# Performance work log

Hardware: AMD Instinct MI355X
Metric: run time of the kernel (lower is better)

The kernel has to match this reference:

```python
import jax, jax.numpy as jnp
import numpy as np

B, NV, L, NKG = 8, 100, 128, 923
NT = NV + 1 + NKG  # 1024 total nodes
DV, DK, DH, H, NLAYERS, VOCAB = 2048, 300, 1024, 8, 3, 50265
DHD = DH // H


def _ln(x, g, b, eps=1e-5):
    m = x.mean(-1, keepdims=True)
    v = x.var(-1, keepdims=True)
    return (x - m) / jnp.sqrt(v + eps) * g + b


def _gat_layer(x, mask, W, bb, a_src, a_dst, ln_g, ln_b):
    # x: [B,N,D], mask: [B,N,N] bool
    Bn, N, D = x.shape
    h = (x @ W + bb).reshape(Bn, N, H, DHD)
    s = jnp.einsum('bnhd,hd->bnh', h, a_src)  # source term
    t = jnp.einsum('bnhd,hd->bnh', h, a_dst)  # target term
    e = jax.nn.leaky_relu(s[:, :, None, :] + t[:, None, :, :], 0.2)  # [B,N,N,H]
    e = jnp.where(mask[..., None], e, -1e9)
    a = jax.nn.softmax(e, axis=2)  # over neighbors j
    out = jnp.einsum('bijh,bjhd->bihd', a, h).reshape(Bn, N, D)
    return _ln(x + out, ln_g, ln_b)


def setup_inputs() -> dict:
    key = jax.random.key(0)
    ks = jax.random.split(key, 24)
    s = 0.02
    inp = {
        'visual_features': jax.random.normal(ks[0], (B, NV, DV), jnp.float32),
        'question_input_ids': jax.random.randint(ks[1], (B, L), 0, VOCAB, jnp.int64) if False else jax.random.randint(ks[1], (B, L), 0, VOCAB).astype(jnp.int32),
        'question_attention_mask': jnp.ones((B, L), jnp.int32),
        'graph_node_features': jax.random.normal(ks[2], (B, NKG, DK), jnp.float32),
        'graph_adj': jax.random.randint(ks[3], (B, NT, NT), 0, 2).astype(jnp.int32),
        'graph_node_types': jax.random.randint(ks[4], (B, NT), 0, 3).astype(jnp.int32),
        # params
        'vis_W': jax.random.normal(ks[5], (DV, DH), jnp.float32) * s,
        'vis_b': jnp.zeros((DH,), jnp.float32),
        'vis_ln_g': jnp.ones((DH,), jnp.float32),
        'vis_ln_b': jnp.zeros((DH,), jnp.float32),
        'tok_emb': jax.random.normal(ks[6], (VOCAB, DH), jnp.float32) * s,
        'q_W': jax.random.normal(ks[7], (DH, DH), jnp.float32) * s,
        'q_b': jnp.zeros((DH,), jnp.float32),
        'q_ln_g': jnp.ones((DH,), jnp.float32),
        'q_ln_b': jnp.zeros((DH,), jnp.float32),
        'kg_W': jax.random.normal(ks[8], (DK, DH), jnp.float32) * s,
        'kg_b': jnp.zeros((DH,), jnp.float32),
        'kg_ln_g': jnp.ones((DH,), jnp.float32),
        'kg_ln_b': jnp.zeros((DH,), jnp.float32),
        'type_emb': jax.random.normal(ks[9], (3, DH), jnp.float32) * s,
        'gat_W': jax.random.normal(ks[10], (NLAYERS, DH, DH), jnp.float32) * s,
        'gat_b': jnp.zeros((NLAYERS, DH), jnp.float32),
        'a_src': jax.random.normal(ks[11], (NLAYERS, H, DHD), jnp.float32) * s,
        'a_dst': jax.random.normal(ks[12], (NLAYERS, H, DHD), jnp.float32) * s,
        'gat_ln_g': jnp.ones((NLAYERS, DH), jnp.float32),
        'gat_ln_b': jnp.zeros((NLAYERS, DH), jnp.float32),
        'readout_W': jax.random.normal(ks[13], (DH, 1), jnp.float32) * s,
        'readout_b': jnp.zeros((1,), jnp.float32),
        'cs_W1': jax.random.normal(ks[14], (DH, DH), jnp.float32) * s,
        'cs_b1': jnp.zeros((DH,), jnp.float32),
        'cs_W2': jax.random.normal(ks[15], (DH, 1), jnp.float32) * s,
        'cs_b2': jnp.zeros((1,), jnp.float32),
    }
    return inp


def reference(visual_features, question_input_ids, question_attention_mask,
              graph_node_features, graph_adj, graph_node_types,
              vis_W, vis_b, vis_ln_g, vis_ln_b,
              tok_emb, q_W, q_b, q_ln_g, q_ln_b,
              kg_W, kg_b, kg_ln_g, kg_ln_b,
              type_emb, gat_W, gat_b, a_src, a_dst, gat_ln_g, gat_ln_b,
              readout_W, readout_b, cs_W1, cs_b1, cs_W2, cs_b2):
    # 1. visual projection
    vis = _ln(visual_features @ vis_W + vis_b, vis_ln_g, vis_ln_b)  # [B,NV,DH]
    # 2. text encoder (embedding + masked mean-pool + proj + LN)
    te = tok_emb[question_input_ids]  # [B,L,DH]
    m = question_attention_mask.astype(te.dtype)[..., None]
    pooled = (te * m).sum(1) / jnp.maximum(m.sum(1), 1.0)
    q = _ln(pooled @ q_W + q_b, q_ln_g, q_ln_b)[:, None, :]  # [B,1,DH]
    # 3. KG projection
    kg = _ln(graph_node_features @ kg_W + kg_b, kg_ln_g, kg_ln_b)
    # 4-5. concat + node-type embeddings
    x = jnp.concatenate([vis, q, kg], axis=1) + type_emb[graph_node_types]
    # 6. dense GAT stack
    mask = graph_adj > 0
    for l in range(NLAYERS):
        x = _gat_layer(x, mask, gat_W[l], gat_b[l], a_src[l], a_dst[l],
                       gat_ln_g[l], gat_ln_b[l])
    # 7. attention-pooled readout
    w = jax.nn.softmax((x @ readout_W + readout_b).squeeze(-1), axis=-1)
    g = (x * w[..., None]).sum(1)  # [B,DH]
    # 8. candidate scorer
    logits = jax.nn.gelu(g @ cs_W1 + cs_b1) @ cs_W2 + cs_b2  # [B,1]
    return logits
```

## Files before the change

kernel.cpp:

```cpp
#include <hip/hip_runtime.h>
#include <math.h>

#define NB 8
#define NV 100
#define LQ 128
#define NKG 923
#define NT 1024
#define DV 2048
#define DK 300
#define DH 1024
#define NH 8
#define DHD 128
#define NLAYERS 3

typedef __attribute__((ext_vector_type(8))) short short8;
typedef __attribute__((ext_vector_type(4))) float f32x4;

__device__ __forceinline__ short f2bf(float f) {
    unsigned u = __float_as_uint(f);
    u += 0x7fff + ((u >> 16) & 1);
    return (short)(u >> 16);
}
__device__ __forceinline__ float bf2f(short s) {
    unsigned u = ((unsigned)(unsigned short)s) << 16;
    return __uint_as_float(u);
}
__device__ __forceinline__ unsigned pack2(float a, float b) {
    return (unsigned)(unsigned short)f2bf(a) | ((unsigned)(unsigned short)f2bf(b) << 16);
}

#if __has_builtin(__builtin_amdgcn_global_load_lds)
#define HAVE_GLL 1
__device__ __forceinline__ void gll16(const void* g, void* l) {
    __builtin_amdgcn_global_load_lds(
        (const __attribute__((address_space(1))) void*)g,
        (__attribute__((address_space(3))) void*)l, 16, 0, 0);
}
#else
#define HAVE_GLL 0
#endif

__device__ __forceinline__ float block_sum1(float a, float* red4) {
#pragma unroll
    for (int off = 32; off > 0; off >>= 1) a += __shfl_xor(a, off, 64);
    int w = threadIdx.x >> 6;
    if ((threadIdx.x & 63) == 0) red4[w] = a;
    __syncthreads();
    return red4[0] + red4[1] + red4[2] + red4[3];
}
__device__ __forceinline__ float block_max1(float a, float* red4) {
#pragma unroll
    for (int off = 32; off > 0; off >>= 1) a = fmaxf(a, __shfl_xor(a, off, 64));
    int w = threadIdx.x >> 6;
    if ((threadIdx.x & 63) == 0) red4[w] = a;
    __syncthreads();
    return fmaxf(fmaxf(red4[0], red4[1]), fmaxf(red4[2], red4[3]));
}
__device__ __forceinline__ float2 block_sum2(float a, float b, float* red8) {
#pragma unroll
    for (int off = 32; off > 0; off >>= 1) {
        a += __shfl_xor(a, off, 64);
        b += __shfl_xor(b, off, 64);
    }
    int w = threadIdx.x >> 6;
    if ((threadIdx.x & 63) == 0) { red8[w] = a; red8[4 + w] = b; }
    __syncthreads();
    float2 r;
    r.x = red8[0] + red8[1] + red8[2] + red8[3];
    r.y = red8[4] + red8[5] + red8[6] + red8[7];
    return r;
}

__global__ __launch_bounds__(256) void bitmask_kernel(
    const int* __restrict__ adj, unsigned* __restrict__ mb)
{
    int bi = blockIdx.x;
    int tid = threadIdx.x;
#pragma unroll
    for (int p = 0; p < 4; ++p) {
        int j = p * 256 + tid;
        unsigned long long bal = __ballot(adj[(size_t)bi * NT + j] > 0);
        if ((tid & 63) == 0) {
            int w = (p * 256 + (tid & 0xC0)) >> 5;
            mb[(size_t)bi * 32 + w]     = (unsigned)bal;
            mb[(size_t)bi * 32 + w + 1] = (unsigned)(bal >> 32);
        }
    }
}

__global__ __launch_bounds__(256) void transpose_cast(
    const float* __restrict__ in, short* __restrict__ out,
    int K, int N, int Kp, size_t in_stride, size_t out_stride)
{
    __shared__ float ls[64][65];
    const float* inL = in + (size_t)blockIdx.z * in_stride;
    short* outL = out + (size_t)blockIdx.z * out_stride;
    int n0 = blockIdx.x * 64, k0 = blockIdx.y * 64;
    int tid = threadIdx.x;
    int j4 = (tid & 15) * 4;
#pragma unroll
    for (int s = 0; s < 4; ++s) {
        int i = (tid >> 4) + s * 16;
        int k = k0 + i;
        float4 v = make_float4(0.f, 0.f, 0.f, 0.f);
        if (k < K) v = *(const float4*)(inL + (size_t)k * N + n0 + j4);
        ls[i][j4 + 0] = v.x; ls[i][j4 + 1] = v.y;
        ls[i][j4 + 2] = v.z; ls[i][j4 + 3] = v.w;
    }
    __syncthreads();
#pragma unroll
    for (int s = 0; s < 4; ++s) {
        int a = (tid >> 4) + s * 16;
        int b = (tid & 15) * 4;
        uint2 pk;
        pk.x = pack2(ls[b + 0][a], ls[b + 1][a]);
        pk.y = pack2(ls[b + 2][a], ls[b + 3][a]);
        *(uint2*)(outL + (size_t)(n0 + a) * Kp + k0 + b) = pk;
    }
}

__global__ __launch_bounds__(256) void gemm_bias_mfma(
    const float* __restrict__ A, const short* __restrict__ Wt,
    const float* __restrict__ bias, float* __restrict__ C,
    int M, int N, int K, int Kp, int ldA)
{
    __shared__ short At[128][32];
    __shared__ short Bt[128][32];
    int tid = threadIdx.x;
    int row0 = blockIdx.y * 128, col0 = blockIdx.x * 128;
    int lane = tid & 63, wave = tid >> 6;
    int quad = lane >> 4, lq = lane & 15;
    int wm = (wave >> 1) * 64, wn = (wave & 1) * 64;
    f32x4 acc[4][4];
#pragma unroll
    for (int i = 0; i < 4; ++i)
#pragma unroll
        for (int j = 0; j < 4; ++j) {
            f32x4 z = {0.f, 0.f, 0.f, 0.f};
            acc[i][j] = z;
        }
    int ar = tid >> 2;
    int ac = (tid & 3) * 8;
    for (int k0 = 0; k0 < Kp; k0 += 32) {
        bool fullk = (k0 + 32 <= K);
#pragma unroll
        for (int s = 0; s < 2; ++s) {
            int r = ar + s * 64;
            int grow = row0 + r;
            short8 pk;
            if (grow < M && fullk) {
                const float* src = A + (size_t)grow * ldA + k0 + ac;
                float4 v0 = *(const float4*)(src);
                float4 v1 = *(const float4*)(src + 4);
                pk[0] = f2bf(v0.x); pk[1] = f2bf(v0.y);
                pk[2] = f2bf(v0.z); pk[3] = f2bf(v0.w);
                pk[4] = f2bf(v1.x); pk[5] = f2bf(v1.y);
                pk[6] = f2bf(v1.z); pk[7] = f2bf(v1.w);
            } else {
#pragma unroll
                for (int e = 0; e < 8; ++e) {
                    int k = k0 + ac + e;
                    pk[e] = (grow < M && k < K)
                          ? f2bf(A[(size_t)grow * ldA + k]) : (short)0;
                }
            }
            *(short8*)&At[r][ac] = pk;
        }
#pragma unroll
        for (int s = 0; s < 2; ++s) {
            int n = ar + s * 64;
            short8 w = *(const short8*)(Wt + (size_t)(col0 + n) * Kp + k0 + ac);
            *(short8*)&Bt[n][ac] = w;
        }
        __syncthreads();
        short8 af[4], bfr[4];
#pragma unroll
        for (int i = 0; i < 4; ++i)
            af[i] = *(short8*)&At[wm + i * 16 + lq][quad * 8];
#pragma unroll
        for (int j = 0; j < 4; ++j)
            bfr[j] = *(short8*)&Bt[wn + j * 16 + lq][quad * 8];
#pragma unroll
        for (int i = 0; i < 4; ++i)
#pragma unroll
            for (int j = 0; j < 4; ++j)
                acc[i][j] = __builtin_amdgcn_mfma_f32_16x16x32_bf16(
                    af[i], bfr[j], acc[i][j], 0, 0, 0);
        __syncthreads();
    }
#pragma unroll
    for (int j = 0; j < 4; ++j) {
        int n = col0 + wn + j * 16 + lq;
        float bv = bias[n];
#pragma unroll
        for (int i = 0; i < 4; ++i) {
#pragma unroll
            for (int r = 0; r < 4; ++r) {
                int m = row0 + wm + i * 16 + quad * 4 + r;
                if (m < M) C[(size_t)m * N + n] = acc[i][j][r] + bv;
            }
        }
    }
}

__global__ __launch_bounds__(256) void gemm_st_mfma(
    const short* __restrict__ Ab, const short* __restrict__ Wt,
    const float* __restrict__ bias,
    const float* __restrict__ asrc, const float* __restrict__ adst,
    short* __restrict__ ht,
    float* __restrict__ sbuf, float* __restrict__ tbuf)
{
    __shared__ __align__(16) short smem[17408];
    short (*At)[32]  = (short(*)[32])smem;
    short (*Bt)[32]  = (short(*)[32])(smem + 4096);
    short (*ct)[136] = (short(*)[136])smem;
    __shared__ float sred[2][128], tred[2][128];
    __shared__ float asl[128], adl[128];
    int tid = threadIdx.x;
    int h = blockIdx.x;
    int row0 = blockIdx.y * 128, col0 = h * 128;
    int b = row0 >> 10, i0 = row0 & 1023;
    int lane = tid & 63, wave = tid >> 6;
    int quad = lane >> 4, lq = lane & 15;
    int wm = (wave >> 1) * 64, wn = (wave & 1) * 64;
    if (tid < 128) asl[tid] = asrc[h * DHD + tid];
    else adl[tid - 128] = adst[h * DHD + tid - 128];
    f32x4 acc[4][4];
#pragma unroll
    for (int i = 0; i < 4; ++i)
#pragma unroll
        for (int j = 0; j < 4; ++j) {
            f32x4 z = {0.f, 0.f, 0.f, 0.f};
            acc[i][j] = z;
        }

    const short* gA0 = Ab + (size_t)(row0 + wave * 16 + (lane >> 2)) * DH + (lane & 3) * 8;
    const short* gA1 = gA0 + (size_t)64 * DH;
    const short* gB0 = Wt + (size_t)(col0 + wave * 16 + (lane >> 2)) * DH + (lane & 3) * 8;
    const short* gB1 = gB0 + (size_t)64 * DH;
#if HAVE_GLL
    char* lA0 = (char*)At + wave * 1024; char* lA1 = lA0 + 4096;
    char* lB0 = (char*)Bt + wave * 1024; char* lB1 = lB0 + 4096;
#endif
    for (int k0 = 0; k0 < DH; k0 += 32) {
#if HAVE_GLL
        gll16(gA0 + k0, lA0); gll16(gA1 + k0, lA1);
        gll16(gB0 + k0, lB0); gll16(gB1 + k0, lB1);
#else
        {
            short8 va0 = *(const short8*)(gA0 + k0);
            short8 va1 = *(const short8*)(gA1 + k0);
            short8 vb0 = *(const short8*)(gB0 + k0);
            short8 vb1 = *(const short8*)(gB1 + k0);
            *(short8*)((char*)At + wave * 1024 + lane * 16) = va0;
            *(short8*)((char*)At + 4096 + wave * 1024 + lane * 16) = va1;
            *(short8*)((char*)Bt + wave * 1024 + lane * 16) = vb0;
            *(short8*)((char*)Bt + 4096 + wave * 1024 + lane * 16) = vb1;
        }
#endif
        __syncthreads();
        short8 af[4], bfr[4];
#pragma unroll
        for (int i = 0; i < 4; ++i)
            af[i] = *(short8*)&At[wm + i * 16 + lq][quad * 8];
#pragma unroll
        for (int j = 0; j < 4; ++j)
            bfr[j] = *(short8*)&Bt[wn + j * 16 + lq][quad * 8];
#pragma unroll
        for (int i = 0; i < 4; ++i)
#pragma unroll
            for (int j = 0; j < 4; ++j)
                acc[i][j] = __builtin_amdgcn_mfma_f32_16x16x32_bf16(
                    af[i], bfr[j], acc[i][j], 0, 0, 0);
        __syncthreads();
    }
#pragma unroll
    for (int j = 0; j < 4; ++j) {
        int d = wn + j * 16 + lq;
        float bv = bias[col0 + d];
#pragma unroll
        for (int i2 = 0; i2 < 4; ++i2) {
            int m = wm + i2 * 16 + quad * 4;
            uint2 pk;
            pk.x = pack2(acc[i2][j][0] + bv, acc[i2][j][1] + bv);
            pk.y = pack2(acc[i2][j][2] + bv, acc[i2][j][3] + bv);
            *(uint2*)&ct[d][m] = pk;
        }
    }
    __syncthreads();
    {
        int d = tid >> 1, half = tid & 1;
        short* dst = ht + ((size_t)(b * NH + h) * DHD + d) * NT + i0 + half * 64;
        const short* src = &ct[d][half * 64];
#pragma unroll
        for (int q = 0; q < 8; ++q)
            *(short8*)(dst + q * 8) = *(const short8*)(src + q * 8);
    }
    {
        int i = tid >> 1, half = tid & 1;
        float sa = 0.f, ta = 0.f;
#pragma unroll 16
        for (int dd = 0; dd < 64; ++dd) {
            int d = half * 64 + dd;
            float hv = bf2f(ct[d][i]);
            sa += hv * asl[d];
            ta += hv * adl[d];
        }
        sred[half][i] = sa; tred[half][i] = ta;
    }
    __syncthreads();
    if (tid < 128) {
        size_t idx = (size_t)(b * NH + h) * NT + i0 + tid;
        sbuf[idx] = sred[0][tid] + sred[1][tid];
        tbuf[idx] = tred[0][tid] + tred[1][tid];
    }
}

__global__ __launch_bounds__(256) void ln_scatter(
    const float* __restrict__ src, float* __restrict__ x,
    const float* __restrict__ g, const float* __restrict__ bta,
    const int* __restrict__ types, const float* __restrict__ type_emb,
    short* __restrict__ xb,
    int rows, int npb, int node_off)
{
    __shared__ float red[8];
    int r = blockIdx.x;
    if (r >= rows) return;
    int tid = threadIdx.x;
    int b = r / npb, n = r - b * npb;
    int node = b * NT + node_off + n;
    float4 v = *(const float4*)(src + (size_t)r * DH + tid * 4);
    float s = v.x + v.y + v.z + v.w;
    float sq = v.x * v.x + v.y * v.y + v.z * v.z + v.w * v.w;
    float2 t2 = block_sum2(s, sq, red);
    float mean = t2.x * (1.0f / DH);
    float var = t2.y * (1.0f / DH) - mean * mean;
    float rstd = 1.0f / sqrtf(var + 1e-5f);
    float4 gv = *(const float4*)(g + tid * 4);
    float4 bv = *(const float4*)(bta + tid * 4);
    int ty = types[node];
    float4 tv = *(const float4*)(type_emb + (size_t)ty * DH + tid * 4);
    float4 o;
    o.x = (v.x - mean) * rstd * gv.x + bv.x + tv.x;
    o.y = (v.y - mean) * rstd * gv.y + bv.y + tv.y;
    o.z = (v.z - mean) * rstd * gv.z + bv.z + tv.z;
    o.w = (v.w - mean) * rstd * gv.w + bv.w + tv.w;
    *(float4*)(x + (size_t)node * DH + tid * 4) = o;
    uint2 pk;
    pk.x = pack2(o.x, o.y);
    pk.y = pack2(o.z, o.w);
    *(uint2*)(xb + (size_t)node * DH + tid * 4) = pk;
}

__global__ __launch_bounds__(256) void ln_residual(
    float* __restrict__ x, const float* __restrict__ o,
    const float* __restrict__ g, const float* __restrict__ bta,
    short* __restrict__ xb,
    const float* __restrict__ rW, const float* __restrict__ rb,
    float* __restrict__ scores)
{
    __shared__ float red[12];
    int r = blockIdx.x;
    int tid = threadIdx.x;
    float* xr = x + (size_t)r * DH;
    float4 xv = *(float4*)(xr + tid * 4);
    float4 ov = *(const float4*)(o + (size_t)r * DH + tid * 4);
    float v0 = xv.x + ov.x, v1 = xv.y + ov.y, v2 = xv.z + ov.z, v3 = xv.w + ov.w;
    float s = v0 + v1 + v2 + v3;
    float sq = v0 * v0 + v1 * v1 + v2 * v2 + v3 * v3;
    float2 t2 = block_sum2(s, sq, red);
    float mean = t2.x * (1.0f / DH);
    float var = t2.y * (1.0f / DH) - mean * mean;
    float rstd = 1.0f / sqrtf(var + 1e-5f);
    float4 gv = *(const float4*)(g + tid * 4);
    float4 bv = *(const float4*)(bta + tid * 4);
    float4 out;
    out.x = (v0 - mean) * rstd * gv.x + bv.x;
    out.y = (v1 - mean) * rstd * gv.y + bv.y;
    out.z = (v2 - mean) * rstd * gv.z + bv.z;
    out.w = (v3 - mean) * rstd * gv.w + bv.w;
    *(float4*)(xr + tid * 4) = out;
    uint2 pk;
    pk.x = pack2(out.x, out.y);
    pk.y = pack2(out.z, out.w);
    *(uint2*)(xb + (size_t)r * DH + tid * 4) = pk;
    if (scores) {
        float4 wv = *(const float4*)(rW + tid * 4);
        float p = out.x * wv.x + out.y * wv.y + out.z * wv.z + out.w * wv.w;
        float totp = block_sum1(p, red + 8);
        if (tid == 0) scores[r] = totp + rb[0];
    }
}

__global__ __launch_bounds__(256) void qproj_fused(
    const float* __restrict__ tok_emb, const int* __restrict__ ids,
    const int* __restrict__ amask, const short* __restrict__ wt_q,
    const float* __restrict__ qb, const float* __restrict__ g,
    const float* __restrict__ bta, const int* __restrict__ types,
    const float* __restrict__ type_emb, float* __restrict__ x,
    short* __restrict__ xb)
{
    __shared__ float pws[4][DH];
    __shared__ float pl[DH];
    __shared__ float pden4[4];
    __shared__ float red[8];
    int b = blockIdx.x, tid = threadIdx.x;
    int wv = tid >> 6, lane = tid & 63;
    float pa[4][4] = {};
    float denom = 0.f;
    for (int i = 0; i < 32; ++i) {
        int l = wv * 32 + i;
        int id = ids[b * LQ + l];
        float m = (float)amask[b * LQ + l];
        denom += m;
        const float* er = tok_emb + (size_t)id * DH + lane * 4;
#pragma unroll
        for (int gg = 0; gg < 4; ++gg) {
            float4 e = *(const float4*)(er + gg * 256);
            pa[gg][0] += m * e.x; pa[gg][1] += m * e.y;
            pa[gg][2] += m * e.z; pa[gg][3] += m * e.w;
        }
    }
#pragma unroll
    for (int gg = 0; gg < 4; ++gg)
        *(float4*)&pws[wv][gg * 256 + lane * 4] =
            make_float4(pa[gg][0], pa[gg][1], pa[gg][2], pa[gg][3]);
    if (lane == 0) pden4[wv] = denom;
    __syncthreads();
    {
        float dtot = pden4[0] + pden4[1] + pden4[2] + pden4[3];
        float inv = 1.0f / fmaxf(dtot, 1.0f);
        int d0 = tid * 4;
        float4 s0 = *(const float4*)&pws[0][d0];
        float4 s1 = *(const float4*)&pws[1][d0];
        float4 s2 = *(const float4*)&pws[2][d0];
        float4 s3 = *(const float4*)&pws[3][d0];
        pl[d0 + 0] = (s0.x + s1.x + s2.x + s3.x) * inv;
        pl[d0 + 1] = (s0.y + s1.y + s2.y + s3.y) * inv;
        pl[d0 + 2] = (s0.z + s1.z + s2.z + s3.z) * inv;
        pl[d0 + 3] = (s0.w + s1.w + s2.w + s3.w) * inv;
    }
    __syncthreads();
    const short* w0 = wt_q + (size_t)(tid * 4 + 0) * DH;
    const short* w1 = wt_q + (size_t)(tid * 4 + 1) * DH;
    const short* w2 = wt_q + (size_t)(tid * 4 + 2) * DH;
    const short* w3 = wt_q + (size_t)(tid * 4 + 3) * DH;
    float o0 = 0, o1 = 0, o2 = 0, o3 = 0;
    for (int k0 = 0; k0 < DH; k0 += 8) {
        float4 p0 = *(const float4*)&pl[k0];
        float4 p1 = *(const float4*)&pl[k0 + 4];
        float pk[8] = {p0.x, p0.y, p0.z, p0.w, p1.x, p1.y, p1.z, p1.w};
        short8 q0 = *(const short8*)(w0 + k0);
        short8 q1 = *(const short8*)(w1 + k0);
        short8 q2 = *(const short8*)(w2 + k0);
        short8 q3 = *(const short8*)(w3 + k0);
#pragma unroll
        for (int e = 0; e < 8; ++e) {
            o0 += pk[e] * bf2f(q0[e]);
            o1 += pk[e] * bf2f(q1[e]);
            o2 += pk[e] * bf2f(q2[e]);
            o3 += pk[e] * bf2f(q3[e]);
        }
    }
    o0 += qb[tid * 4 + 0]; o1 += qb[tid * 4 + 1];
    o2 += qb[tid * 4 + 2]; o3 += qb[tid * 4 + 3];
    float s = o0 + o1 + o2 + o3;
    float sq = o0 * o0 + o1 * o1 + o2 * o2 + o3 * o3;
    float2 t2 = block_sum2(s, sq, red);
    float mean = t2.x * (1.0f / DH);
    float var = t2.y * (1.0f / DH) - mean * mean;
    float rstd = 1.0f / sqrtf(var + 1e-5f);
    float4 gv = *(const float4*)(g + tid * 4);
    float4 bv = *(const float4*)(bta + tid * 4);
    int node = b * NT + NV;
    int ty = types[node];
    float4 tv = *(const float4*)(type_emb + (size_t)ty * DH + tid * 4);
    float4 o;
    o.x = (o0 - mean) * rstd * gv.x + bv.x + tv.x;
    o.y = (o1 - mean) * rstd * gv.y + bv.y + tv.y;
    o.z = (o2 - mean) * rstd * gv.z + bv.z + tv.z;
    o.w = (o3 - mean) * rstd * gv.w + bv.w + tv.w;
    *(float4*)(x + (size_t)node * DH + tid * 4) = o;
    uint2 pk2;
    pk2.x = pack2(o.x, o.y);
    pk2.y = pack2(o.z, o.w);
    *(uint2*)(xb + (size_t)node * DH + tid * 4) = pk2;
}

__global__ __launch_bounds__(256) void agg_mfma(
    const short* __restrict__ ht, const unsigned* __restrict__ mb,
    const float* __restrict__ s, const float* __restrict__ t,
    float* __restrict__ obuf)
{
    __shared__ __align__(16) short vt[128 * 64];
    __shared__ short at[64][72];
    __shared__ unsigned mrow[64][32];
    __shared__ float sv[64], alpha_s[64], lfin[64];
    int i0 = blockIdx.x * 64;
    int h = blockIdx.y, b = blockIdx.z;
    int tid = threadIdx.x;
    int lane = tid & 63, wave = tid >> 6;
    int quad = lane >> 4, lq = lane & 15;
    int wi = (wave >> 1) * 32;
    int wd = (wave & 1) * 64;
    if (tid < 64) sv[tid] = s[(size_t)(b * NH + h) * NT + i0 + tid];
#pragma unroll
    for (int s2 = 0; s2 < 2; ++s2) {
        int f = tid + s2 * 256;
        int ii2 = f >> 3, w4 = (f & 7) * 4;
        *(uint4*)&mrow[ii2][w4] =
            *(const uint4*)(mb + ((size_t)(b * NT + i0 + ii2)) * 32 + w4);
    }
    const float* tptr = t + (size_t)(b * NH + h) * NT;
    const short* hbase = ht + ((size_t)(b * NH + h) * DHD) * NT;
    const short* gsrc[4];
    char* ldst[4];
#pragma unroll
    for (int s2 = 0; s2 < 4; ++s2) {
        int f = tid + s2 * 256;
        int d = f >> 3, cc = f & 7;
        gsrc[s2] = hbase + (size_t)d * NT + ((cc ^ (d & 7)) * 8);
        ldst[s2] = (char*)vt + wave * 1024 + s2 * 4096;
    }
    f32x4 acc[2][4];
#pragma unroll
    for (int i = 0; i < 2; ++i)
#pragma unroll
        for (int j = 0; j < 4; ++j) {
            f32x4 z = {0.f, 0.f, 0.f, 0.f};
            acc[i][j] = z;
        }
    int ii = tid >> 2;
    int jq = (tid & 3) * 16;
    float m_run = -3e38f, l_run = 0.f;
    for (int j0 = 0; j0 < NT; j0 += 64) {
        __syncthreads();
#if HAVE_GLL
#pragma unroll
        for (int s2 = 0; s2 < 4; ++s2) gll16(gsrc[s2] + j0, ldst[s2]);
#else
#pragma unroll
        for (int s2 = 0; s2 < 4; ++s2) {
            int f = tid + s2 * 256;
            short8 v8 = *(const short8*)(gsrc[s2] + j0);
            *(short8*)((char*)vt + (size_t)f * 16) = v8;
        }
#endif
        float vv[16];
        unsigned mw;
        float tmax = -3e38f;
        {
            mw = mrow[ii][(j0 + jq) >> 5] >> ((j0 + jq) & 31);
            float svv = sv[ii];
            float4 t0 = *(const float4*)(tptr + j0 + jq);
            float4 t1 = *(const float4*)(tptr + j0 + jq + 4);
            float4 t2 = *(const float4*)(tptr + j0 + jq + 8);
            float4 t3 = *(const float4*)(tptr + j0 + jq + 12);
            float tv16[16] = {t0.x, t0.y, t0.z, t0.w, t1.x, t1.y, t1.z, t1.w,
                              t2.x, t2.y, t2.z, t2.w, t3.x, t3.y, t3.z, t3.w};
#pragma unroll
            for (int e = 0; e < 16; ++e) {
                float v = svv + tv16[e];
                v = v > 0.f ? v : 0.2f * v;
                v = ((mw >> e) & 1) ? v : -1e9f;
                vv[e] = v;
                tmax = fmaxf(tmax, v);
            }
        }
        tmax = fmaxf(tmax, __shfl_xor(tmax, 1, 64));
        tmax = fmaxf(tmax, __shfl_xor(tmax, 2, 64));
        float m_new = fmaxf(m_run, tmax);
        float al = __expf(m_run - m_new);
        float tsum = 0.f;
        short8 p0, p1;
#pragma unroll
        for (int e = 0; e < 8; ++e) {
            float w = ((mw >> e) & 1) ? __expf(vv[e] - m_new) : 0.f;
            tsum += w; p0[e] = f2bf(w);
        }
#pragma unroll
        for (int e = 0; e < 8; ++e) {
            float w = ((mw >> (8 + e)) & 1) ? __expf(vv[8 + e] - m_new) : 0.f;
            tsum += w; p1[e] = f2bf(w);
        }
        tsum += __shfl_xor(tsum, 1, 64);
        tsum += __shfl_xor(tsum, 2, 64);
        l_run = l_run * al + tsum;
        m_run = m_new;
        *(short8*)&at[ii][jq] = p0;
        *(short8*)&at[ii][jq + 8] = p1;
        if ((tid & 3) == 0) alpha_s[ii] = al;
        __syncthreads();
#pragma unroll
        for (int i2 = 0; i2 < 2; ++i2)
#pragma unroll
            for (int r = 0; r < 4; ++r) {
                float arow = alpha_s[wi + i2 * 16 + quad * 4 + r];
#pragma unroll
                for (int j = 0; j < 4; ++j) acc[i2][j][r] *= arow;
            }
        const char* vtb = (const char*)vt;
#pragma unroll
        for (int ks = 0; ks < 2; ++ks) {
            short8 af[2], bfr[4];
            af[0] = *(short8*)&at[wi + lq][ks * 32 + quad * 8];
            af[1] = *(short8*)&at[wi + 16 + lq][ks * 32 + quad * 8];
            int cc = ks * 4 + quad;
            int sx = (cc ^ (lq & 7)) * 16;
#pragma unroll
            for (int j = 0; j < 4; ++j)
                bfr[j] = *(const short8*)(vtb + (wd + j * 16 + lq) * 128 + sx);
#pragma unroll
            for (int i2 = 0; i2 < 2; ++i2)
#pragma unroll
                for (int j = 0; j < 4; ++j)
                    acc[i2][j] = __builtin_amdgcn_mfma_f32_16x16x32_bf16(
                        af[i2], bfr[j], acc[i2][j], 0, 0, 0);
        }
    }
    if ((tid & 3) == 0) lfin[ii] = l_run;
    __syncthreads();
#pragma unroll
    for (int i2 = 0; i2 < 2; ++i2) {
#pragma unroll
        for (int r = 0; r < 4; ++r) {
            int il = wi + i2 * 16 + quad * 4 + r;
            float inv = 1.0f / lfin[il];
            float* dst = obuf + ((size_t)(b * NT + i0 + il)) * DH + h * DHD + wd;
#pragma unroll
            for (int j = 0; j < 4; ++j)
                dst[j * 16 + lq] = acc[i2][j][r] * inv;
        }
    }
}

__global__ __launch_bounds__(256) void pool_part(
    const float* __restrict__ x, const float* __restrict__ scores,
    float* __restrict__ gpart)
{
    __shared__ float red[8];
    int p = blockIdx.x;
    int b = blockIdx.y;
    int tid = threadIdx.x;
    const float* sr = scores + (size_t)b * NT;
    float v[4];
    float mx = -3e38f;
#pragma unroll
    for (int k = 0; k < 4; ++k) { v[k] = sr[tid + k * 256]; mx = fmaxf(mx, v[k]); }
    float m = block_max1(mx, red);
    float ls = 0.f;
#pragma unroll
    for (int k = 0; k < 4; ++k) ls += expf(v[k] - m);
    float tot = block_sum1(ls, red + 4);
    float inv = 1.0f / tot;
    float a0 = 0, a1 = 0, a2 = 0, a3 = 0;
    for (int n = p * 128; n < (p + 1) * 128; ++n) {
        float wv = expf(sr[n] - m) * inv;
        float4 xv = *(const float4*)(x + ((size_t)(b * NT + n)) * DH + tid * 4);
        a0 += wv * xv.x; a1 += wv * xv.y; a2 += wv * xv.z; a3 += wv * xv.w;
    }
    float4 o = make_float4(a0, a1, a2, a3);
    *(float4*)(gpart + ((size_t)(b * 8 + p)) * DH + tid * 4) = o;
}

__global__ __launch_bounds__(256) void scorer_part(
    const float* __restrict__ gpart, const float* __restrict__ W1,
    float* __restrict__ spart)
{
    __shared__ float gsh[128];
    int c = blockIdx.x, b = blockIdx.y;
    int tid = threadIdx.x;
    if (tid < 128) {
        int d = c * 128 + tid;
        float gv = 0.f;
#pragma unroll
        for (int p = 0; p < 8; ++p) gv += gpart[((size_t)(b * 8 + p)) * DH + d];
        gsh[tid] = gv;
    }
    __syncthreads();
    float acc[4] = {};
    for (int dd = 0; dd < 128; ++dd) {
        float gv = gsh[dd];
        const float* wr = W1 + (size_t)(c * 128 + dd) * DH;
#pragma unroll
        for (int cc = 0; cc < 4; ++cc) acc[cc] += gv * wr[tid + cc * 256];
    }
#pragma unroll
    for (int cc = 0; cc < 4; ++cc)
        spart[((size_t)(b * 8 + c)) * DH + tid + cc * 256] = acc[cc];
}
__global__ __launch_bounds__(256) void scorer_fin(
    const float* __restrict__ spart, const float* __restrict__ b1,
    const float* __restrict__ W2, const float* __restrict__ b2,
    float* __restrict__ out)
{
    __shared__ float red[4];
    int b = blockIdx.x;
    int tid = threadIdx.x;
    float part = 0.f;
#pragma unroll
    for (int cc = 0; cc < 4; ++cc) {
        int k = tid + cc * 256;
        float s = 0.f;
#pragma unroll
        for (int c = 0; c < 8; ++c) s += spart[((size_t)(b * 8 + c)) * DH + k];
        float u = s + b1[k];
        float inner = 0.7978845608028654f * (u + 0.044715f * u * u * u);
        float gel = 0.5f * u * (1.0f + tanhf(inner));
        part += gel * W2[k];
    }
    float tot = block_sum1(part, red);
    if (tid == 0) out[b] = tot + b2[0];
}

extern "C" void kernel_launch(void* const* d_in, const int* in_sizes, int n_in,
                              void* d_out, int out_size, void* d_ws, size_t ws_size,
                              hipStream_t stream)
{
    const float* visual   = (const float*)d_in[0];
    const int*   q_ids    = (const int*)d_in[1];
    const int*   q_mask   = (const int*)d_in[2];
    const float* kg_feat  = (const float*)d_in[3];
    const int*   adj      = (const int*)d_in[4];
    const int*   ntypes   = (const int*)d_in[5];
    const float* vis_W    = (const float*)d_in[6];
    const float* vis_b    = (const float*)d_in[7];
    const float* vis_lng  = (const float*)d_in[8];
    const float* vis_lnb  = (const float*)d_in[9];
    const float* tok_emb  = (const float*)d_in[10];
    const float* q_W      = (const float*)d_in[11];
    const float* q_b      = (const float*)d_in[12];
    const float* q_lng    = (const float*)d_in[13];
    const float* q_lnb    = (const float*)d_in[14];
    const float* kg_W     = (const float*)d_in[15];
    const float* kg_b     = (const float*)d_in[16];
    const float* kg_lng   = (const float*)d_in[17];
    const float* kg_lnb   = (const float*)d_in[18];
    const float* type_emb = (const float*)d_in[19];
    const float* gat_W    = (const float*)d_in[20];
    const float* gat_b    = (const float*)d_in[21];
    const float* a_src    = (const float*)d_in[22];
    const float* a_dst    = (const float*)d_in[23];
    const float* gat_lng  = (const float*)d_in[24];
    const float* gat_lnb  = (const float*)d_in[25];
    const float* read_W   = (const float*)d_in[26];
    const float* read_b   = (const float*)d_in[27];
    const float* cs_W1    = (const float*)d_in[28];
    const float* cs_b1    = (const float*)d_in[29];
    const float* cs_W2    = (const float*)d_in[30];
    const float* cs_b2    = (const float*)d_in[31];
    float* out = (float*)d_out;

    float* ws = (float*)d_ws;
    const size_t NROW = (size_t)NB * NT;
    float* x      = ws;
    float* obuf   = x + NROW * DH;
    float* sbuf   = obuf + NROW * DH;
    float* tbuf   = sbuf + NB * NH * NT;
    float* pooled = tbuf + NB * NH * NT;
    float* scores = pooled + NB * DH;
    float* gpart  = scores + NROW;
    float* ppool  = gpart + NB * 8 * DH;
    float* pden   = ppool + NB * 4 * DH;
    float* spart  = pden + 64;
    short* wt_gat = (short*)(spart + NB * 8 * DH);
    short* ht     = wt_gat + (size_t)NLAYERS * DH * DH;
    unsigned* mb  = (unsigned*)(ht + (size_t)NB * NH * DHD * NT);
    short* xb     = (short*)(mb + (size_t)NB * NT * 32);
    short* wt_vis = xb + NROW * DH;
    short* wt_q   = wt_vis + (size_t)1024 * 2048;
    short* wt_kg  = wt_q + (size_t)1024 * 1024;

    transpose_cast<<<dim3(16, 32, 1), 256, 0, stream>>>(vis_W, wt_vis, DV, DH, DV, 0, 0);
    transpose_cast<<<dim3(16, 16, 1), 256, 0, stream>>>(q_W, wt_q, DH, DH, DH, 0, 0);
    transpose_cast<<<dim3(16, 5, 1), 256, 0, stream>>>(kg_W, wt_kg, DK, DH, 320, 0, 0);
    transpose_cast<<<dim3(16, 16, NLAYERS), 256, 0, stream>>>(
        gat_W, wt_gat, DH, DH, DH, (size_t)DH * DH, (size_t)DH * DH);
    bitmask_kernel<<<NB * NT, 256, 0, stream>>>(adj, mb);

    gemm_bias_mfma<<<dim3(8, 7), 256, 0, stream>>>(
        visual, wt_vis, vis_b, obuf, NB * NV, DH, DV, DV, DV);
    ln_scatter<<<NB * NV, 256, 0, stream>>>(obuf, x, vis_lng, vis_lnb,
        ntypes, type_emb, xb, NB * NV, NV, 0);

    qproj_fused<<<NB, 256, 0, stream>>>(tok_emb, q_ids, q_mask, wt_q,
        q_b, q_lng, q_lnb, ntypes, type_emb, x, xb);

    gemm_bias_mfma<<<dim3(8, 58), 256, 0, stream>>>(
        kg_feat, wt_kg, kg_b, obuf, NB * NKG, DH, DK, 320, DK);
    ln_scatter<<<NB * NKG, 256, 0, stream>>>(obuf, x, kg_lng, kg_lnb,
        ntypes, type_emb, xb, NB * NKG, NKG, NV + 1);

    for (int l = 0; l < NLAYERS; ++l) {
        const float* bl  = gat_b + (size_t)l * DH;
        const float* asl = a_src + (size_t)l * NH * DHD;
        const float* adl = a_dst + (size_t)l * NH * DHD;
        gemm_st_mfma<<<dim3(NH, 64), 256, 0, stream>>>(
            xb, wt_gat + (size_t)l * DH * DH, bl, asl, adl, ht, sbuf, tbuf);
        agg_mfma<<<dim3(16, NH, NB), 256, 0, stream>>>(
            ht, mb, sbuf, tbuf, obuf);
        ln_residual<<<NB * NT, 256, 0, stream>>>(x, obuf,
            gat_lng + (size_t)l * DH, gat_lnb + (size_t)l * DH, xb,
            read_W, read_b, (l == NLAYERS - 1) ? scores : nullptr);
    }

    pool_part<<<dim3(8, NB), 256, 0, stream>>>(x, scores, gpart);
    scorer_part<<<dim3(8, NB), 256, 0, stream>>>(gpart, cs_W1, spart);
    scorer_fin<<<NB, 256, 0, stream>>>(spart, cs_b1, cs_W2, cs_b2, out);
}
```

Before: 959.5 us.

## Double agg_mfma row tile to 128 and remap blocks for XCD-local head reuse

The GAT aggregation kernel now processes 128 query rows per block instead of 64, so each value tile loaded into shared memory feeds twice as many MFMAs and the V/t streaming traffic is halved. Each thread handles two softmax rows with separate running max/sum, and the accumulator grows to 4x4 fragments. Block ids are remapped so blocks sharing the same (batch, head) land on the same XCD, improving L2 reuse of the head's V data. Costs are higher register and LDS use and half as many blocks (512), which may reduce occupancy.

Measured after the change: 979.9 us. 1.02x slower.

```diff
diff --git a/kernel.cpp b/kernel.cpp
--- a/kernel.cpp
+++ b/kernel.cpp
@@ -493,23 +493,26 @@
     float* __restrict__ obuf)
 {
     __shared__ __align__(16) short vt[128 * 64];
-    __shared__ short at[64][72];
-    __shared__ unsigned mrow[64][32];
-    __shared__ float sv[64], alpha_s[64], lfin[64];
-    int i0 = blockIdx.x * 64;
-    int h = blockIdx.y, b = blockIdx.z;
+    __shared__ short at[128][72];
+    __shared__ unsigned mrow[128][32];
+    __shared__ float sv[128], alpha_s[128], lfin[128];
+    int lid = blockIdx.x + 8 * (blockIdx.y + NH * blockIdx.z);
+    int xcd = lid & 7, k = lid >> 3;
+    int p = xcd + 8 * (k & 7);
+    int h = p & 7, b = p >> 3;
+    int i0 = (k >> 3) * 128;
     int tid = threadIdx.x;
     int lane = tid & 63, wave = tid >> 6;
     int quad = lane >> 4, lq = lane & 15;
-    int wi = (wave >> 1) * 32;
+    int wi = (wave >> 1) * 64;
     int wd = (wave & 1) * 64;
-    if (tid < 64) sv[tid] = s[(size_t)(b * NH + h) * NT + i0 + tid];
-#pragma unroll
-    for (int s2 = 0; s2 < 2; ++s2) {
+    if (tid < 128) sv[tid] = s[(size_t)(b * NH + h) * NT + i0 + tid];
+#pragma unroll
+    for (int s2 = 0; s2 < 4; ++s2) {
         int f = tid + s2 * 256;
-        int ii2 = f >> 3, w4 = (f & 7) * 4;
-        *(uint4*)&mrow[ii2][w4] =
-            *(const uint4*)(mb + ((size_t)(b * NT + i0 + ii2)) * 32 + w4);
+        int r = f >> 3, w4 = (f & 7) * 4;
+        *(uint4*)&mrow[r][w4] =
+            *(const uint4*)(mb + ((size_t)(b * NT + i0 + r)) * 32 + w4);
     }
     const float* tptr = t + (size_t)(b * NH + h) * NT;
     const short* hbase = ht + ((size_t)(b * NH + h) * DHD) * NT;
@@ -522,9 +525,9 @@
         gsrc[s2] = hbase + (size_t)d * NT + ((cc ^ (d & 7)) * 8);
         ldst[s2] = (char*)vt + wave * 1024 + s2 * 4096;
     }
-    f32x4 acc[2][4];
-#pragma unroll
-    for (int i = 0; i < 2; ++i)
+    f32x4 acc[4][4];
+#pragma unroll
+    for (int i = 0; i < 4; ++i)
 #pragma unroll
         for (int j = 0; j < 4; ++j) {
             f32x4 z = {0.f, 0.f, 0.f, 0.f};
@@ -532,7 +535,8 @@
         }
     int ii = tid >> 2;
     int jq = (tid & 3) * 16;
-    float m_run = -3e38f, l_run = 0.f;
+    float m_run[2] = {-3e38f, -3e38f};
+    float l_run[2] = {0.f, 0.f};
     for (int j0 = 0; j0 < NT; j0 += 64) {
         __syncthreads();
 #if HAVE_GLL
@@ -546,18 +550,19 @@
             *(short8*)((char*)vt + (size_t)f * 16) = v8;
         }
 #endif
-        float vv[16];
-        unsigned mw;
-        float tmax = -3e38f;
-        {
-            mw = mrow[ii][(j0 + jq) >> 5] >> ((j0 + jq) & 31);
-            float svv = sv[ii];
-            float4 t0 = *(const float4*)(tptr + j0 + jq);
-            float4 t1 = *(const float4*)(tptr + j0 + jq + 4);
-            float4 t2 = *(const float4*)(tptr + j0 + jq + 8);
-            float4 t3 = *(const float4*)(tptr + j0 + jq + 12);
-            float tv16[16] = {t0.x, t0.y, t0.z, t0.w, t1.x, t1.y, t1.z, t1.w,
-                              t2.x, t2.y, t2.z, t2.w, t3.x, t3.y, t3.z, t3.w};
+        float4 t0 = *(const float4*)(tptr + j0 + jq);
+        float4 t1 = *(const float4*)(tptr + j0 + jq + 4);
+        float4 t2 = *(const float4*)(tptr + j0 + jq + 8);
+        float4 t3 = *(const float4*)(tptr + j0 + jq + 12);
+        float tv16[16] = {t0.x, t0.y, t0.z, t0.w, t1.x, t1.y, t1.z, t1.w,
+                          t2.x, t2.y, t2.z, t2.w, t3.x, t3.y, t3.z, t3.w};
+#pragma unroll
+        for (int r2 = 0; r2 < 2; ++r2) {
+            int row = ii + r2 * 64;
+            unsigned mw = mrow[row][(j0 + jq) >> 5] >> ((j0 + jq) & 31);
+            float svv = sv[row];
+            float vv[16];
+            float tmax = -3e38f;
 #pragma unroll
             for (int e = 0; e < 16; ++e) {
                 float v = svv + tv16[e];
@@ -566,33 +571,33 @@
                 vv[e] = v;
                 tmax = fmaxf(tmax, v);
             }
-        }
-        tmax = fmaxf(tmax, __shfl_xor(tmax, 1, 64));
-        tmax = fmaxf(tmax, __shfl_xor(tmax, 2, 64));
-        float m_new = fmaxf(m_run, tmax);
-        float al = __expf(m_run - m_new);
-        float tsum = 0.f;
-        short8 p0, p1;
-#pragma unroll
-        for (int e = 0; e < 8; ++e) {
-            float w = ((mw >> e) & 1) ? __expf(vv[e] - m_new) : 0.f;
-            tsum += w; p0[e] = f2bf(w);
-        }
-#pragma unroll
-        for (int e = 0; e < 8; ++e) {
-            float w = ((mw >> (8 + e)) & 1) ? __expf(vv[8 + e] - m_new) : 0.f;
-            tsum += w; p1[e] = f2bf(w);
-        }
-        tsum += __shfl_xor(tsum, 1, 64);
-        tsum += __shfl_xor(tsum, 2, 64);
-        l_run = l_run * al + tsum;
-        m_run = m_new;
-        *(short8*)&at[ii][jq] = p0;
-        *(short8*)&at[ii][jq + 8] = p1;
-        if ((tid & 3) == 0) alpha_s[ii] = al;
+            tmax = fmaxf(tmax, __shfl_xor(tmax, 1, 64));
+            tmax = fmaxf(tmax, __shfl_xor(tmax, 2, 64));
+            float m_new = fmaxf(m_run[r2], tmax);
+            float al = __expf(m_run[r2] - m_new);
+            float tsum = 0.f;
+            short8 p0, p1;
+#pragma unroll
+            for (int e = 0; e < 8; ++e) {
+                float w = ((mw >> e) & 1) ? __expf(vv[e] - m_new) : 0.f;
+                tsum += w; p0[e] = f2bf(w);
+            }
+#pragma unroll
+            for (int e = 0; e < 8; ++e) {
+                float w = ((mw >> (8 + e)) & 1) ? __expf(vv[8 + e] - m_new) : 0.f;
+                tsum += w; p1[e] = f2bf(w);
+            }
+            tsum += __shfl_xor(tsum, 1, 64);
+            tsum += __shfl_xor(tsum, 2, 64);
+            l_run[r2] = l_run[r2] * al + tsum;
+            m_run[r2] = m_new;
+            *(short8*)&at[row][jq] = p0;
+            *(short8*)&at[row][jq + 8] = p1;
+            if ((tid & 3) == 0) alpha_s[row] = al;
+        }
         __syncthreads();
 #pragma unroll
-        for (int i2 = 0; i2 < 2; ++i2)
+        for (int i2 = 0; i2 < 4; ++i2)
 #pragma unroll
             for (int r = 0; r < 4; ++r) {
                 float arow = alpha_s[wi + i2 * 16 + quad * 4 + r];
@@ -602,26 +607,27 @@
         const char* vtb = (const char*)vt;
 #pragma unroll
         for (int ks = 0; ks < 2; ++ks) {
-            short8 af[2], bfr[4];
-            af[0] = *(short8*)&at[wi + lq][ks * 32 + quad * 8];
-            af[1] = *(short8*)&at[wi + 16 + lq][ks * 32 + quad * 8];
+            short8 af[4], bfr[4];
+#pragma unroll
+            for (int i2 = 0; i2 < 4; ++i2)
+                af[i2] = *(short8*)&at[wi + i2 * 16 + lq][ks * 32 + quad * 8];
             int cc = ks * 4 + quad;
             int sx = (cc ^ (lq & 7)) * 16;
 #pragma unroll
             for (int j = 0; j < 4; ++j)
                 bfr[j] = *(const short8*)(vtb + (wd + j * 16 + lq) * 128 + sx);
 #pragma unroll
-            for (int i2 = 0; i2 < 2; ++i2)
+            for (int i2 = 0; i2 < 4; ++i2)
 #pragma unroll
                 for (int j = 0; j < 4; ++j)
                     acc[i2][j] = __builtin_amdgcn_mfma_f32_16x16x32_bf16(
                         af[i2], bfr[j], acc[i2][j], 0, 0, 0);
         }
     }
-    if ((tid & 3) == 0) lfin[ii] = l_run;
-    __syncthreads();
-#pragma unroll
-    for (int i2 = 0; i2 < 2; ++i2) {
+    if ((tid & 3) == 0) { lfin[ii] = l_run[0]; lfin[ii + 64] = l_run[1]; }
+    __syncthreads();
+#pragma unroll
+    for (int i2 = 0; i2 < 4; ++i2) {
 #pragma unroll
         for (int r = 0; r < 4; ++r) {
             int il = wi + i2 * 16 + quad * 4 + r;
@@ -797,7 +803,7 @@
         const float* adl = a_dst + (size_t)l * NH * DHD;
         gemm_st_mfma<<<dim3(NH, 64), 256, 0, stream>>>(
             xb, wt_gat + (size_t)l * DH * DH, bl, asl, adl, ht, sbuf, tbuf);
-        agg_mfma<<<dim3(16, NH, NB), 256, 0, stream>>>(
+        agg_mfma<<<dim3(8, NH, NB), 256, 0, stream>>>(
             ht, mb, sbuf, tbuf, obuf);
         ln_residual<<<NB * NT, 256, 0, stream>>>(x, obuf,
             gat_lng + (size_t)l * DH, gat_lnb + (size_t)l * DH, xb,
```
